# Optimization experiments

Hardware: AMD Instinct MI355X
Metric: run time of the kernel (lower is better)

## Reference

```python
import jax, jax.numpy as jnp
import numpy as np

D_MODEL = 512

def setup_inputs() -> dict:
    key = jax.random.key(0)
    k1, k2, k3, k4, k5 = jax.random.split(key, 5)
    x = jax.random.normal(k1, (8, D_MODEL, 2048), dtype=jnp.float32)
    s = 1.0 / np.sqrt(D_MODEL)
    W_qkv = jax.random.uniform(k2, (D_MODEL, 3 * D_MODEL), dtype=jnp.float32, minval=-s, maxval=s)
    b_qkv = jax.random.uniform(k3, (3 * D_MODEL,), dtype=jnp.float32, minval=-s, maxval=s)
    W_proj = jax.random.uniform(k4, (D_MODEL, D_MODEL), dtype=jnp.float32, minval=-s, maxval=s)
    b_proj = jax.random.uniform(k5, (D_MODEL,), dtype=jnp.float32, minval=-s, maxval=s)
    return {"x": x, "W_qkv": W_qkv, "b_qkv": b_qkv, "W_proj": W_proj, "b_proj": b_proj}

def reference(x, W_qkv, b_qkv, W_proj, b_proj):
    # x: [B, L, N] with L == d_model; attend across the N variable axis
    xt = jnp.swapaxes(x, 1, 2)                      # [B, N, L]
    L = xt.shape[-1]
    qkv = xt @ W_qkv + b_qkv                        # [B, N, 3L]
    q, k, v = jnp.split(qkv, 3, axis=-1)            # each [B, N, L]
    attn = jnp.einsum('bnd,bmd->bnm', q, k) / jnp.sqrt(jnp.float32(L))
    attn = jax.nn.softmax(attn, axis=-1)            # [B, N, N]
    out = jnp.einsum('bnm,bmd->bnd', attn, v)       # [B, N, L]
    out = out @ W_proj + b_proj                     # [B, N, L]
    return jnp.swapaxes(out, 1, 2)                  # [B, L, N]
```

## Files before the change

### kernel.cpp

```cpp
#include <hip/hip_runtime.h>

#define NVAR 2048
#define DM   512
#define J3   1536

typedef _Float16 f16;
typedef _Float16 f16x8 __attribute__((ext_vector_type(8)));
typedef _Float16 f16x4 __attribute__((ext_vector_type(4)));
typedef float    f32x4 __attribute__((ext_vector_type(4)));

#define GLOAD(gp, lp) __builtin_amdgcn_global_load_lds( \
    (const __attribute__((address_space(1))) void*)(gp), \
    (__attribute__((address_space(3))) void*)(lp), 16, 0, 0)

__global__ __launch_bounds__(256)
void k_tr(const float* __restrict__ src, f16* __restrict__ dst,
          int R, int C, long bsSrc, long bsDst) {
    __shared__ float t[64][65];
    const float* s = src + (size_t)blockIdx.z * bsSrc;
    f16* d = dst + (size_t)blockIdx.z * bsDst;
    const int c0 = blockIdx.x * 64, r0 = blockIdx.y * 64;
    const int tx = threadIdx.x & 63, w = threadIdx.x >> 6;
#pragma unroll
    for (int i = 0; i < 16; ++i) {
        int r = w * 16 + i;
        t[r][tx] = s[(size_t)(r0 + r) * C + c0 + tx];
    }
    __syncthreads();
#pragma unroll
    for (int i = 0; i < 16; ++i) {
        int c = w * 16 + i;
        d[(size_t)(c0 + c) * R + r0 + tx] = (f16)t[tx][c];
    }
}

template<int MODE>
__global__ __launch_bounds__(512, 2)
void gemm_big(const f16* __restrict__ A, const f16* __restrict__ B,
              long bsA, long bsB, int lda, int ldb, int K, int nbx,
              const float* __restrict__ bias, float scale,
              f16* __restrict__ o0, f16* __restrict__ o1, f16* __restrict__ o2) {
    __shared__ f16 sA[256 * 64];
    __shared__ f16 sB[256 * 64];
    const int tid  = threadIdx.x;
    const int lane = tid & 63;
    const int w    = __builtin_amdgcn_readfirstlane(tid >> 6);
    const int wm   = (w >> 2) * 128;
    const int wn   = (w & 3) * 64;
    const int z    = blockIdx.x;
    const int bid  = blockIdx.y;
    const int bxA  = bid % nbx;
    const int bxB  = bid / nbx;

    const f16* Ab = A + (size_t)z * bsA + (size_t)bxA * 256 * lda;
    const f16* Bb = B + (size_t)z * bsB + (size_t)bxB * 256 * ldb;

    int srcA[4], srcB[4];
#pragma unroll
    for (int i = 0; i < 4; ++i) {
        int slot = i * 512 + tid;
        int row  = slot >> 3;
        int s    = (slot & 7) ^ (row & 7);
        srcA[i] = row * lda + s * 8;
        srcB[i] = row * ldb + s * 8;
    }

    int koff[2];
#pragma unroll
    for (int ks = 0; ks < 2; ++ks)
        koff[ks] = ((ks * 4 + (lane >> 4)) ^ (lane & 7)) * 8;
    const int rowA = (wm + (lane & 15)) * 64;
    const int rowB = (wn + (lane & 15)) * 64;

    f32x4 acc[8][4] = {};

    for (int k0 = 0; k0 < K; k0 += 64) {
        __syncthreads();
#pragma unroll
        for (int i = 0; i < 4; ++i)
            GLOAD(Ab + srcA[i] + k0, sA + i * 4096 + w * 512);
#pragma unroll
        for (int i = 0; i < 4; ++i)
            GLOAD(Bb + srcB[i] + k0, sB + i * 4096 + w * 512);
        __syncthreads();

        f16x8 bv[4][2];
#pragma unroll
        for (int nj = 0; nj < 4; ++nj)
#pragma unroll
            for (int ks = 0; ks < 2; ++ks)
                bv[nj][ks] = *(const f16x8*)(sB + rowB + nj * 1024 + koff[ks]);
#pragma unroll
        for (int h = 0; h < 2; ++h) {
            f16x8 av[4][2];
#pragma unroll
            for (int mi = 0; mi < 4; ++mi)
#pragma unroll
                for (int ks = 0; ks < 2; ++ks)
                    av[mi][ks] = *(const f16x8*)(sA + rowA + (h * 4 + mi) * 1024 + koff[ks]);
#pragma unroll
            for (int mi = 0; mi < 4; ++mi)
#pragma unroll
                for (int nj = 0; nj < 4; ++nj)
#pragma unroll
                    for (int ks = 0; ks < 2; ++ks)
                        acc[h * 4 + mi][nj] = __builtin_amdgcn_mfma_f32_16x16x32_f16(
                            av[mi][ks], bv[nj][ks], acc[h * 4 + mi][nj], 0, 0, 0);
        }
    }

    const int rb0 = bxA * 256 + wm + (lane >> 4) * 4;
    const int cb0 = bxB * 256 + wn + (lane & 15);

    if (MODE == 0) {
        const int seg = (bxA * 256) >> 9;
#pragma unroll
        for (int mi = 0; mi < 8; ++mi) {
            const int j = rb0 + mi * 16;
            const f32x4 b4 = *(const f32x4*)(bias + j);
#pragma unroll
            for (int nj = 0; nj < 4; ++nj) {
                const int n = cb0 + nj * 16;
                if (seg == 2) {
#pragma unroll
                    for (int r = 0; r < 4; ++r)
                        o2[((size_t)z * DM + (j - 1024 + r)) * NVAR + n] =
                            (f16)(acc[mi][nj][r] + b4[r]);
                } else {
                    f16* dst = seg ? o1 : o0;
                    const int jj = seg ? j - 512 : j;
                    f16x4 vv;
#pragma unroll
                    for (int r = 0; r < 4; ++r) vv[r] = (f16)(acc[mi][nj][r] + b4[r]);
                    *(f16x4*)(dst + ((size_t)z * NVAR + n) * DM + jj) = vv;
                }
            }
        }
    } else {
#pragma unroll
        for (int mi = 0; mi < 8; ++mi)
#pragma unroll
            for (int nj = 0; nj < 4; ++nj) {
                f16x4 vv;
#pragma unroll
                for (int r = 0; r < 4; ++r)
                    vv[r] = (f16)__expf(acc[mi][nj][r] * scale);
                *(f16x4*)(o0 + ((size_t)z * NVAR + cb0 + nj * 16) * NVAR
                               + rb0 + mi * 16) = vv;
            }
    }
}

template<int MODE>
__global__ __launch_bounds__(256)
void gemm_f16(const f16* __restrict__ A, const f16* __restrict__ B,
              long bsA, long bsB, int lda, int ldb, int K, int nbx,
              const float* __restrict__ bias, float scale,
              f16* __restrict__ o0, float* __restrict__ of) {
    __shared__ f16 sA[128 * 64];
    __shared__ f16 sB[128 * 64];
    const int tid  = threadIdx.x;
    const int lane = tid & 63;
    const int w    = __builtin_amdgcn_readfirstlane(tid >> 6);
    const int wm   = (w >> 1) * 64;
    const int wn   = (w & 1) * 64;
    const int z    = blockIdx.x;
    const int bid  = blockIdx.y;
    const int bxA  = bid % nbx;
    const int bxB  = bid / nbx;

    const f16* Ab = A + (size_t)z * bsA + (size_t)bxA * 128 * lda;
    const f16* Bb = B + (size_t)z * bsB + (size_t)bxB * 128 * ldb;

    int srcA[4], srcB[4];
#pragma unroll
    for (int i = 0; i < 4; ++i) {
        int slot = i * 256 + tid;
        int row  = slot >> 3;
        int s    = (slot & 7) ^ (row & 7);
        srcA[i] = row * lda + s * 8;
        srcB[i] = row * ldb + s * 8;
    }

    f16x8 ones;
#pragma unroll
    for (int e = 0; e < 8; ++e) ones[e] = (f16)1.0f;

    f32x4 acc[4][4] = {};
    f32x4 accrs[4] = {};

    for (int k0 = 0; k0 < K; k0 += 64) {
        __syncthreads();
#pragma unroll
        for (int i = 0; i < 4; ++i) {
            GLOAD(Ab + srcA[i] + k0, sA + i * 2048 + w * 512);
            GLOAD(Bb + srcB[i] + k0, sB + i * 2048 + w * 512);
        }
        __syncthreads();
#pragma unroll
        for (int kh = 0; kh < 2; ++kh) {
            f16x8 av[4], bv[4];
#pragma unroll
            for (int mi = 0; mi < 4; ++mi) {
                int r = wm + mi * 16 + (lane & 15);
                int s = (kh * 4 + (lane >> 4)) ^ (r & 7);
                av[mi] = *(const f16x8*)(sA + r * 64 + s * 8);
            }
#pragma unroll
            for (int nj = 0; nj < 4; ++nj) {
                int r = wn + nj * 16 + (lane & 15);
                int s = (kh * 4 + (lane >> 4)) ^ (r & 7);
                bv[nj] = *(const f16x8*)(sB + r * 64 + s * 8);
            }
            if constexpr (MODE == 2) {
#pragma unroll
                for (int nj = 0; nj < 4; ++nj)
                    accrs[nj] = __builtin_amdgcn_mfma_f32_16x16x32_f16(
                        ones, bv[nj], accrs[nj], 0, 0, 0);
            }
#pragma unroll
            for (int mi = 0; mi < 4; ++mi)
#pragma unroll
                for (int nj = 0; nj < 4; ++nj)
                    acc[mi][nj] = __builtin_amdgcn_mfma_f32_16x16x32_f16(
                        av[mi], bv[nj], acc[mi][nj], 0, 0, 0);
        }
    }

    const int rb0 = bxA * 128 + wm + (lane >> 4) * 4;
    const int cb0 = bxB * 128 + wn + (lane & 15);

    if (MODE == 2) {
        float inv[4];
#pragma unroll
        for (int nj = 0; nj < 4; ++nj) inv[nj] = 1.0f / accrs[nj][0];
#pragma unroll
        for (int mi = 0; mi < 4; ++mi)
#pragma unroll
            for (int nj = 0; nj < 4; ++nj) {
                f16x4 vv;
#pragma unroll
                for (int r = 0; r < 4; ++r)
                    vv[r] = (f16)(acc[mi][nj][r] * inv[nj]);
                *(f16x4*)(o0 + ((size_t)z * NVAR + cb0 + nj * 16) * DM
                               + rb0 + mi * 16) = vv;
            }
    } else {
#pragma unroll
        for (int mi = 0; mi < 4; ++mi)
#pragma unroll
            for (int nj = 0; nj < 4; ++nj) {
                const int l = cb0 + nj * 16;
                const float bb = bias[l];
                f32x4 vv;
#pragma unroll
                for (int r = 0; r < 4; ++r) vv[r] = acc[mi][nj][r] + bb;
                *(f32x4*)(of + ((size_t)z * DM + l) * NVAR + rb0 + mi * 16) = vv;
            }
    }
}

extern "C" void kernel_launch(void* const* d_in, const int* in_sizes, int n_in,
                              void* d_out, int out_size, void* d_ws, size_t ws_size,
                              hipStream_t stream) {
    const float* x     = (const float*)d_in[0];
    const float* Wqkv  = (const float*)d_in[1];
    const float* bqkv  = (const float*)d_in[2];
    const float* Wproj = (const float*)d_in[3];
    const float* bproj = (const float*)d_in[4];
    float* out = (float*)d_out;

    const size_t PB = (size_t)NVAR * DM;
    f16* xT  = (f16*)d_ws;
    f16* q   = xT + 8 * PB;
    f16* kk  = q  + 8 * PB;
    f16* vT  = kk + 8 * PB;
    f16* S   = vT + 8 * PB;
    f16* O   = S  + (size_t)8 * NVAR * NVAR;
    f16* WqT = O  + 8 * PB;
    f16* WpT = WqT + (size_t)J3 * DM;

    k_tr<<<dim3(NVAR / 64, DM / 64, 8), 256, 0, stream>>>(
        x, xT, DM, NVAR, (long)DM * NVAR, (long)NVAR * DM);
    k_tr<<<dim3(J3 / 64, DM / 64, 1), 256, 0, stream>>>(Wqkv, WqT, DM, J3, 0, 0);
    k_tr<<<dim3(DM / 64, DM / 64, 1), 256, 0, stream>>>(Wproj, WpT, DM, DM, 0, 0);

    gemm_big<0><<<dim3(8, 6 * 8), 512, 0, stream>>>(
        WqT, xT, 0, (long)NVAR * DM, DM, DM, DM, 6,
        bqkv, 1.f, q, kk, vT);

    gemm_big<1><<<dim3(8, 8 * 8), 512, 0, stream>>>(
        kk, q, (long)NVAR * DM, (long)NVAR * DM, DM, DM, DM, 8,
        nullptr, 0.044194173824159216f, S, nullptr, nullptr);

    gemm_f16<2><<<dim3(8, 4 * 16), 256, 0, stream>>>(
        vT, S, (long)DM * NVAR, (long)NVAR * NVAR, NVAR, NVAR, NVAR, 4,
        nullptr, 1.f, O, nullptr);

    gemm_f16<3><<<dim3(8, 16 * 4), 256, 0, stream>>>(
        O, WpT, (long)NVAR * DM, 0, DM, DM, DM, 16,
        bproj, 1.f, nullptr, out);
}
```

Before: 185.5 us.

## Move QKV projection to 128-tile GEMM and vectorize transpose kernel

The QKV projection GEMM moves from the 256x256-tile, 512-thread kernel to the 128x128-tile, 256-thread kernel with the bias and split epilogue moved across, which quadruples the block count from 384 to 1536 for better CU fill. The transpose kernel now uses float4 global loads and f16x4 global stores instead of scalar accesses. In exchange, the smaller tiles reuse less data per block, and the column reads from LDS in the transpose may hit more bank conflicts.

Measured after the change: 184.1 us. Within noise of the previous version (-0.7%).

```diff
diff --git a/kernel.cpp b/kernel.cpp
--- a/kernel.cpp
+++ b/kernel.cpp
@@ -20,26 +20,29 @@
     const float* s = src + (size_t)blockIdx.z * bsSrc;
     f16* d = dst + (size_t)blockIdx.z * bsDst;
     const int c0 = blockIdx.x * 64, r0 = blockIdx.y * 64;
-    const int tx = threadIdx.x & 63, w = threadIdx.x >> 6;
-#pragma unroll
-    for (int i = 0; i < 16; ++i) {
-        int r = w * 16 + i;
-        t[r][tx] = s[(size_t)(r0 + r) * C + c0 + tx];
+    const int lx = threadIdx.x & 15, ly = threadIdx.x >> 4;
+#pragma unroll
+    for (int p = 0; p < 4; ++p) {
+        int r = p * 16 + ly;
+        f32x4 v = *(const f32x4*)(s + (size_t)(r0 + r) * C + c0 + lx * 4);
+#pragma unroll
+        for (int i = 0; i < 4; ++i) t[r][lx * 4 + i] = v[i];
     }
     __syncthreads();
 #pragma unroll
-    for (int i = 0; i < 16; ++i) {
-        int c = w * 16 + i;
-        d[(size_t)(c0 + c) * R + r0 + tx] = (f16)t[tx][c];
+    for (int p = 0; p < 4; ++p) {
+        int c = p * 16 + ly;
+        f16x4 h;
+#pragma unroll
+        for (int i = 0; i < 4; ++i) h[i] = (f16)t[lx * 4 + i][c];
+        *(f16x4*)(d + (size_t)(c0 + c) * R + r0 + lx * 4) = h;
     }
 }
 
-template<int MODE>
 __global__ __launch_bounds__(512, 2)
 void gemm_big(const f16* __restrict__ A, const f16* __restrict__ B,
               long bsA, long bsB, int lda, int ldb, int K, int nbx,
-              const float* __restrict__ bias, float scale,
-              f16* __restrict__ o0, f16* __restrict__ o1, f16* __restrict__ o2) {
+              float scale, f16* __restrict__ o0) {
     __shared__ f16 sA[256 * 64];
     __shared__ f16 sB[256 * 64];
     const int tid  = threadIdx.x;
@@ -111,52 +114,26 @@
 
     const int rb0 = bxA * 256 + wm + (lane >> 4) * 4;
     const int cb0 = bxB * 256 + wn + (lane & 15);
-
-    if (MODE == 0) {
-        const int seg = (bxA * 256) >> 9;
-#pragma unroll
-        for (int mi = 0; mi < 8; ++mi) {
-            const int j = rb0 + mi * 16;
-            const f32x4 b4 = *(const f32x4*)(bias + j);
-#pragma unroll
-            for (int nj = 0; nj < 4; ++nj) {
-                const int n = cb0 + nj * 16;
-                if (seg == 2) {
-#pragma unroll
-                    for (int r = 0; r < 4; ++r)
-                        o2[((size_t)z * DM + (j - 1024 + r)) * NVAR + n] =
-                            (f16)(acc[mi][nj][r] + b4[r]);
-                } else {
-                    f16* dst = seg ? o1 : o0;
-                    const int jj = seg ? j - 512 : j;
-                    f16x4 vv;
-#pragma unroll
-                    for (int r = 0; r < 4; ++r) vv[r] = (f16)(acc[mi][nj][r] + b4[r]);
-                    *(f16x4*)(dst + ((size_t)z * NVAR + n) * DM + jj) = vv;
-                }
-            }
-        }
-    } else {
-#pragma unroll
-        for (int mi = 0; mi < 8; ++mi)
-#pragma unroll
-            for (int nj = 0; nj < 4; ++nj) {
-                f16x4 vv;
-#pragma unroll
-                for (int r = 0; r < 4; ++r)
-                    vv[r] = (f16)__expf(acc[mi][nj][r] * scale);
-                *(f16x4*)(o0 + ((size_t)z * NVAR + cb0 + nj * 16) * NVAR
-                               + rb0 + mi * 16) = vv;
-            }
-    }
+#pragma unroll
+    for (int mi = 0; mi < 8; ++mi)
+#pragma unroll
+        for (int nj = 0; nj < 4; ++nj) {
+            f16x4 vv;
+#pragma unroll
+            for (int r = 0; r < 4; ++r)
+                vv[r] = (f16)__expf(acc[mi][nj][r] * scale);
+            *(f16x4*)(o0 + ((size_t)z * NVAR + cb0 + nj * 16) * NVAR
+                           + rb0 + mi * 16) = vv;
+        }
 }
 
 template<int MODE>
 __global__ __launch_bounds__(256)
 void gemm_f16(const f16* __restrict__ A, const f16* __restrict__ B,
               long bsA, long bsB, int lda, int ldb, int K, int nbx,
-              const float* __restrict__ bias, float scale,
-              f16* __restrict__ o0, float* __restrict__ of) {
+              const float* __restrict__ bias,
+              f16* __restrict__ o0, f16* __restrict__ o1, f16* __restrict__ o2,
+              float* __restrict__ of) {
     __shared__ f16 sA[128 * 64];
     __shared__ f16 sB[128 * 64];
     const int tid  = threadIdx.x;
@@ -230,7 +207,31 @@
     const int rb0 = bxA * 128 + wm + (lane >> 4) * 4;
     const int cb0 = bxB * 128 + wn + (lane & 15);
 
-    if (MODE == 2) {
+    if (MODE == 0) {
+        const int seg = (bxA * 128) >> 9;
+#pragma unroll
+        for (int mi = 0; mi < 4; ++mi) {
+            const int j = rb0 + mi * 16;
+            const f32x4 b4 = *(const f32x4*)(bias + j);
+#pragma unroll
+            for (int nj = 0; nj < 4; ++nj) {
+                const int n = cb0 + nj * 16;
+                if (seg == 2) {
+#pragma unroll
+                    for (int r = 0; r < 4; ++r)
+                        o2[((size_t)z * DM + (j - 1024 + r)) * NVAR + n] =
+                            (f16)(acc[mi][nj][r] + b4[r]);
+                } else {
+                    f16* dst = seg ? o1 : o0;
+                    const int jj = seg ? j - 512 : j;
+                    f16x4 vv;
+#pragma unroll
+                    for (int r = 0; r < 4; ++r) vv[r] = (f16)(acc[mi][nj][r] + b4[r]);
+                    *(f16x4*)(dst + ((size_t)z * NVAR + n) * DM + jj) = vv;
+                }
+            }
+        }
+    } else if (MODE == 2) {
         float inv[4];
 #pragma unroll
         for (int nj = 0; nj < 4; ++nj) inv[nj] = 1.0f / accrs[nj][0];
@@ -285,19 +286,19 @@
     k_tr<<<dim3(J3 / 64, DM / 64, 1), 256, 0, stream>>>(Wqkv, WqT, DM, J3, 0, 0);
     k_tr<<<dim3(DM / 64, DM / 64, 1), 256, 0, stream>>>(Wproj, WpT, DM, DM, 0, 0);
 
-    gemm_big<0><<<dim3(8, 6 * 8), 512, 0, stream>>>(
-        WqT, xT, 0, (long)NVAR * DM, DM, DM, DM, 6,
-        bqkv, 1.f, q, kk, vT);
-
-    gemm_big<1><<<dim3(8, 8 * 8), 512, 0, stream>>>(
+    gemm_f16<0><<<dim3(8, 12 * 16), 256, 0, stream>>>(
+        WqT, xT, 0, (long)NVAR * DM, DM, DM, DM, 12,
+        bqkv, q, kk, vT, nullptr);
+
+    gemm_big<<<dim3(8, 8 * 8), 512, 0, stream>>>(
         kk, q, (long)NVAR * DM, (long)NVAR * DM, DM, DM, DM, 8,
-        nullptr, 0.044194173824159216f, S, nullptr, nullptr);
+        0.044194173824159216f, S);
 
     gemm_f16<2><<<dim3(8, 4 * 16), 256, 0, stream>>>(
         vT, S, (long)DM * NVAR, (long)NVAR * NVAR, NVAR, NVAR, NVAR, 4,
-        nullptr, 1.f, O, nullptr);
+        nullptr, O, nullptr, nullptr, nullptr);
 
     gemm_f16<3><<<dim3(8, 16 * 4), 256, 0, stream>>>(
         O, WpT, (long)NVAR * DM, 0, DM, DM, DM, 16,
-        bproj, 1.f, nullptr, out);
+        bproj, nullptr, nullptr, nullptr, out);
 }
```
